# Kernel tuning notes

Measured on AMD Instinct MI355X. Metric: run time of the kernel, lower is better.

The kernel has to match this reference:

```python
import jax, jax.numpy as jnp
import numpy as np

B, C, L, K = 8, 128, 32768, 129  # batch, seq_len (channels), samples, filter length


def setup_inputs() -> dict:
    key = jax.random.key(0)
    k0, k1, k2, k3 = jax.random.split(key, 4)
    return {
        "x": jax.random.normal(k0, (B, C, L), dtype=jnp.float32),
        "weights_mag": jnp.ones((C, 1), dtype=jnp.float32),
        "weights_angle": jax.random.uniform(k1, (C, 1), dtype=jnp.float32),
        "kernel_real": jax.random.normal(k2, (K,), dtype=jnp.float32),
        "kernel_imag": jax.random.normal(k3, (K,), dtype=jnp.float32),
    }


def _matched_filter(x, kr, ki):
    # PyTorch F.conv1d is cross-correlation; mf_coeffs = conj(kernel) repeated per
    # channel (groups = C), so every channel is correlated with the SAME conj kernel.
    # Input is real (x.to(complex64) has zero imag), so:
    #   out = corr(x, conj(k)) = corr(x, kr) - 1j * corr(x, ki)
    b, c, l = x.shape
    kk = kr.shape[0]
    pad = kk // 2
    w = jnp.stack([kr, -ki])[:, None, :]  # [2, 1, K]: real and imag of conj kernel
    y = jax.lax.conv_general_dilated(
        x.reshape(b * c, 1, l), w,
        window_strides=(1,), padding=[(pad, pad)],
        dimension_numbers=("NCH", "OIH", "NCH"),
    )  # [B*C, 2, L]
    yr = y[:, 0].reshape(b, c, l)
    yi = y[:, 1].reshape(b, c, l)
    return yr + 1j * yi  # complex64


def reference(x, weights_mag, weights_angle, kernel_real, kernel_imag):
    batch = x.shape[0]
    y = _matched_filter(x, kernel_real, kernel_imag)          # [B, C, L] complex64
    phase = jnp.arctan(weights_angle)                          # [C, 1]
    norm_mag = batch * jax.nn.softmax(weights_mag, axis=0)     # [C, 1]
    scale = (norm_mag.astype(jnp.complex64) * jnp.exp(-1j * phase))  # [C, 1] complex
    return scale * y
```

## Files before the change

### kernel.cpp

```cpp
#include <hip/hip_runtime.h>
#include <hip/hip_bf16.h>
#include <math.h>

constexpr int Bc = 8, Cc = 128, Lc = 32768, Kc = 129;

constexpr int MLEN = 256;
constexpr int T    = 16;
constexpr int NSEG = Lc / (MLEN * T);
constexpr int WPB  = 4;
constexpr int THREADS = 64 * WPB;
constexpr int LASTCW  = Lc / MLEN - 1;

typedef __attribute__((ext_vector_type(8))) short short8;
typedef __attribute__((ext_vector_type(4))) float floatx4;

#define WAITVM(N) do { asm volatile("s_waitcnt vmcnt(" #N ")" ::: "memory"); \
                       __builtin_amdgcn_sched_barrier(0); } while (0)

__device__ __forceinline__ unsigned short f2bf(float f) {
    return __builtin_bit_cast(unsigned short, __float2bfloat16(f));
}

__device__ __forceinline__ short8 cvt8(const float4& a, const float4& b) {
    __hip_bfloat162 p0 = __float22bfloat162_rn(make_float2(a.x, a.y));
    __hip_bfloat162 p1 = __float22bfloat162_rn(make_float2(a.z, a.w));
    __hip_bfloat162 p2 = __float22bfloat162_rn(make_float2(b.x, b.y));
    __hip_bfloat162 p3 = __float22bfloat162_rn(make_float2(b.z, b.w));
    ushort2 u0, u1, u2, u3;
    __builtin_memcpy(&u0, &p0, 4);
    __builtin_memcpy(&u1, &p1, 4);
    __builtin_memcpy(&u2, &p2, 4);
    __builtin_memcpy(&u3, &p3, 4);
    short8 r;
    r[0] = (short)u0.x; r[1] = (short)u0.y;
    r[2] = (short)u1.x; r[3] = (short)u1.y;
    r[4] = (short)u2.x; r[5] = (short)u2.y;
    r[6] = (short)u3.x; r[7] = (short)u3.y;
    return r;
}

__global__ void scale_kernel(const float* __restrict__ wm,
                             const float* __restrict__ wa,
                             float* __restrict__ ws, int C, float batchf) {
    int c = threadIdx.x;
    if (c >= C) return;
    float m = -1e30f;
    for (int i = 0; i < C; ++i) m = fmaxf(m, wm[i]);
    float s = 0.f;
    for (int i = 0; i < C; ++i) s += expf(wm[i] - m);
    float nm = batchf * expf(wm[c] - m) / s;
    float a = wa[c];
    float inv = rsqrtf(1.f + a * a);
    ws[2 * c]     = nm * inv;
    ws[2 * c + 1] = nm * a * inv;
}

__global__ __launch_bounds__(THREADS, 4)
void mf_kernel(const float* __restrict__ x,
               const float* __restrict__ kr,
               const float* __restrict__ ki,
               const float* __restrict__ sc_ss,
               float* __restrict__ out, int interleaved) {
    __shared__ __align__(16) unsigned short lb[WPB][512];

    const int seg = blockIdx.x;
    const int rg  = blockIdx.y;
    const int tid = threadIdx.x;
    const int lane= tid & 63;
    const int wv  = tid >> 6;
    const int fh  = lane >> 4;
    const int fn  = lane & 15;

    const int row = rg * WPB + wv;
    const int cw0 = seg * T;

    short8 br[5], bi[5];
    #pragma unroll
    for (int d = 0; d < 5; ++d) {
        #pragma unroll
        for (int e = 0; e < 8; ++e) {
            int idx = 32 * d + 8 * fh + e - fn;
            bool ok = (idx >= 0) && (idx < Kc);
            br[d][e] = (short)f2bf(ok ? kr[idx] : 0.f);
            bi[d][e] = (short)f2bf(ok ? ki[idx] : 0.f);
        }
    }

    const int ch = row & (Cc - 1);
    const float scv = sc_ss[2 * ch];
    const float ssv = sc_ss[2 * ch + 1];

    const float* __restrict__ xrow = x + (size_t)row * Lc;

    float4 F[2][2];
    auto ISSUE = [&](int cw, int buf0) {
        int g = cw * MLEN - 64 + 8 * lane;
        g = min(max(g, 0), Lc - 8);
        F[buf0][0] = *reinterpret_cast<const float4*>(xrow + g);
        F[buf0][1] = *reinterpret_cast<const float4*>(xrow + g + 4);
    };

    ISSUE(cw0, 0);
    ISSUE(cw0 + 1, 1);

    #pragma unroll
    for (int c = 0; c < T; ++c) {
        const int cw  = cw0 + c;
        const int buf = c & 1;

        if (c == 0)          WAITVM(2);
        else if (c == T - 1) WAITVM(4);
        else                 WAITVM(6);

        short8 h = cvt8(F[buf][0], F[buf][1]);

        if (c + 2 < T) ISSUE(cw + 2, buf);

        *reinterpret_cast<short8*>(&lb[wv][8 * lane]) = h;

        floatx4 cr = {0.f, 0.f, 0.f, 0.f};
        floatx4 ci = {0.f, 0.f, 0.f, 0.f};
        #pragma unroll
        for (int d = 0; d < 5; ++d) {
            short8 a = *reinterpret_cast<const short8*>(
                &lb[wv][16 * fn + 8 * fh + 32 * d]);
            if (cw == 0) {
                if (2 * fn + fh + 4 * d < 8) a = short8{0,0,0,0,0,0,0,0};
            } else if (cw == LASTCW) {
                if (2 * fn + fh + 4 * d >= 40) a = short8{0,0,0,0,0,0,0,0};
            }
            cr = __builtin_amdgcn_mfma_f32_16x16x32_bf16(a, br[d], cr, 0, 0, 0);
            ci = __builtin_amdgcn_mfma_f32_16x16x32_bf16(a, bi[d], ci, 0, 0, 0);
        }

        if (!interleaved) {
            float* op = out + (size_t)row * Lc + cw * MLEN + 64 * fh + fn;
            #pragma unroll
            for (int r = 0; r < 4; ++r)
                op[16 * r] = scv * cr[r] - ssv * ci[r];
        } else {
            float2* op = reinterpret_cast<float2*>(out) +
                         ((size_t)row * Lc + cw * MLEN + 64 * fh + fn);
            #pragma unroll
            for (int r = 0; r < 4; ++r)
                op[16 * r] = make_float2(scv * cr[r] - ssv * ci[r],
                                         -scv * ci[r] - ssv * cr[r]);
        }
    }
}

extern "C" void kernel_launch(void* const* d_in, const int* in_sizes, int n_in,
                              void* d_out, int out_size, void* d_ws, size_t ws_size,
                              hipStream_t stream) {
    const float* x  = (const float*)d_in[0];
    const float* wm = (const float*)d_in[1];
    const float* wa = (const float*)d_in[2];
    const float* kr = (const float*)d_in[3];
    const float* ki = (const float*)d_in[4];
    float* out = (float*)d_out;
    float* ws  = (float*)d_ws;

    const int C = in_sizes[1];
    const long long N = (long long)Bc * Cc * Lc;
    const int interleaved = (out_size == 2 * N) ? 1 : 0;

    hipLaunchKernelGGL(scale_kernel, dim3(1), dim3(C), 0, stream,
                       wm, wa, ws, C, (float)Bc);

    dim3 grid(NSEG, (Bc * Cc) / WPB);
    hipLaunchKernelGGL(mf_kernel, grid, dim3(THREADS), 0, stream,
                       x, kr, ki, ws, out, interleaved);
}
```

Before: 70.89 us.

## Double-buffer LDS staging and halve chunks per block

```diff
diff --git a/kernel.cpp b/kernel.cpp
--- a/kernel.cpp
+++ b/kernel.cpp
@@ -5,7 +5,7 @@
 constexpr int Bc = 8, Cc = 128, Lc = 32768, Kc = 129;
 
 constexpr int MLEN = 256;
-constexpr int T    = 16;
+constexpr int T    = 8;
 constexpr int NSEG = Lc / (MLEN * T);
 constexpr int WPB  = 4;
 constexpr int THREADS = 64 * WPB;
@@ -61,7 +61,7 @@
                const float* __restrict__ ki,
                const float* __restrict__ sc_ss,
                float* __restrict__ out, int interleaved) {
-    __shared__ __align__(16) unsigned short lb[WPB][512];
+    __shared__ __align__(16) unsigned short lb[WPB][2][512];
 
     const int seg = blockIdx.x;
     const int rg  = blockIdx.y;
@@ -92,38 +92,41 @@
 
     const float* __restrict__ xrow = x + (size_t)row * Lc;
 
-    float4 F[2][2];
-    auto ISSUE = [&](int cw, int buf0) {
+    float4 F[2];
+    auto ISSUE = [&](int cw) {
         int g = cw * MLEN - 64 + 8 * lane;
         g = min(max(g, 0), Lc - 8);
-        F[buf0][0] = *reinterpret_cast<const float4*>(xrow + g);
-        F[buf0][1] = *reinterpret_cast<const float4*>(xrow + g + 4);
+        F[0] = *reinterpret_cast<const float4*>(xrow + g);
+        F[1] = *reinterpret_cast<const float4*>(xrow + g + 4);
     };
 
-    ISSUE(cw0, 0);
-    ISSUE(cw0 + 1, 1);
+    ISSUE(cw0);
+    WAITVM(0);
+    {
+        short8 h = cvt8(F[0], F[1]);
+        *reinterpret_cast<short8*>(&lb[wv][0][8 * lane]) = h;
+    }
+    ISSUE(cw0 + 1);
 
     #pragma unroll
     for (int c = 0; c < T; ++c) {
-        const int cw  = cw0 + c;
-        const int buf = c & 1;
+        const int cw = cw0 + c;
+        const int wb = c & 1;
 
-        if (c == 0)          WAITVM(2);
-        else if (c == T - 1) WAITVM(4);
-        else                 WAITVM(6);
-
-        short8 h = cvt8(F[buf][0], F[buf][1]);
-
-        if (c + 2 < T) ISSUE(cw + 2, buf);
-
-        *reinterpret_cast<short8*>(&lb[wv][8 * lane]) = h;
+        if (c + 1 < T) {
+            if (c == 0) WAITVM(0);
+            else        WAITVM(4);
+            short8 h = cvt8(F[0], F[1]);
+            *reinterpret_cast<short8*>(&lb[wv][wb ^ 1][8 * lane]) = h;
+            if (c + 2 < T) ISSUE(cw + 2);
+        }
 
         floatx4 cr = {0.f, 0.f, 0.f, 0.f};
         floatx4 ci = {0.f, 0.f, 0.f, 0.f};
         #pragma unroll
         for (int d = 0; d < 5; ++d) {
             short8 a = *reinterpret_cast<const short8*>(
-                &lb[wv][16 * fn + 8 * fh + 32 * d]);
+                &lb[wv][wb][16 * fn + 8 * fh + 32 * d]);
             if (cw == 0) {
                 if (2 * fn + fh + 4 * d < 8) a = short8{0,0,0,0,0,0,0,0};
             } else if (cw == LASTCW) {
```

Measured after the change: 81.01 us. 1.14x slower.
